# Optimization experiments

Hardware: AMD Instinct MI355X
Metric: run time of the kernel (lower is better)

Reference implementation:

```python
import jax, jax.numpy as jnp
import numpy as np

B, N, S, F = 16384, 1152, 576, 8  # batch, n_sites, n_symm, features
LOG2 = float(np.log(2.0))


def log_cosh(x):
    # numerically stable log(cosh(x)) = |x| + log1p(exp(-2|x|)) - log(2)
    a = jnp.abs(x)
    return a + jnp.log1p(jnp.exp(-2.0 * a)) - LOG2


def setup_inputs() -> dict:
    key = jax.random.key(0)
    ks = iter(jax.random.split(key, 32))
    f32 = jnp.float32
    d = {}
    d['x'] = jax.random.normal(next(ks), (B, N), dtype=f32)
    d['symmetries'] = jax.random.randint(next(ks), (S, N), 0, N, dtype=jnp.int32)
    d['corr0'] = jax.random.randint(next(ks), (576, 4), 0, N, dtype=jnp.int32)
    d['corr1'] = jax.random.randint(next(ks), (576, 4), 0, N, dtype=jnp.int32)
    d['corr2'] = jax.random.randint(next(ks), (24, 24), 0, N, dtype=jnp.int32)
    d['corr3'] = jax.random.randint(next(ks), (24, 24), 0, N, dtype=jnp.int32)
    d['corr0_symm'] = jax.random.randint(next(ks), (S, 576), 0, 576, dtype=jnp.int32)
    d['corr1_symm'] = jax.random.randint(next(ks), (S, 576), 0, 576, dtype=jnp.int32)
    d['corr2_symm'] = jax.random.randint(next(ks), (S, 24), 0, 24, dtype=jnp.int32)
    d['corr3_symm'] = jax.random.randint(next(ks), (S, 24), 0, 24, dtype=jnp.int32)
    std = 0.01
    d['hidden_bias'] = std * jax.random.normal(next(ks), (F,), dtype=f32)
    d['symm_kernel'] = std * jax.random.normal(next(ks), (F, N), dtype=f32)
    d['visible_bias'] = std * jax.random.normal(next(ks), (2,), dtype=f32)
    d['corr0_bias'] = std * jax.random.normal(next(ks), (1,), dtype=f32)
    d['corr0_kernel'] = std * jax.random.normal(next(ks), (F, 576), dtype=f32)
    d['corr1_bias'] = std * jax.random.normal(next(ks), (1,), dtype=f32)
    d['corr1_kernel'] = std * jax.random.normal(next(ks), (F, 576), dtype=f32)
    d['corr2_bias'] = std * jax.random.normal(next(ks), (1,), dtype=f32)
    d['corr2_kernel'] = std * jax.random.normal(next(ks), (F, 24), dtype=f32)
    d['corr3_bias'] = std * jax.random.normal(next(ks), (1,), dtype=f32)
    d['corr3_kernel'] = std * jax.random.normal(next(ks), (F, 24), dtype=f32)
    d['loop0_hidden_bias'] = std * jax.random.normal(next(ks), (F,), dtype=f32)
    d['loop0_kernel'] = std * jax.random.normal(next(ks), (F, 24), dtype=f32)
    d['loop1_hidden_bias'] = std * jax.random.normal(next(ks), (F,), dtype=f32)
    d['loop1_kernel'] = std * jax.random.normal(next(ks), (F, 24), dtype=f32)
    return d


def reference(x, symmetries, corr0, corr1, corr2, corr3,
              corr0_symm, corr1_symm, corr2_symm, corr3_symm,
              hidden_bias, symm_kernel, visible_bias,
              corr0_bias, corr0_kernel, corr1_bias, corr1_kernel,
              corr2_bias, corr2_kernel, corr3_bias, corr3_kernel,
              loop0_hidden_bias, loop0_kernel, loop1_hidden_bias, loop1_kernel):
    n_batch = x.shape[0]
    # symmetrized kernel: (F, S, N)
    K = jnp.take(symm_kernel, symmetries, axis=1)
    theta = jnp.einsum('bn,fsn->bfs', x, K)  # (B, F, S)
    theta = theta + hidden_bias[:, None]
    bias = jnp.sum(x.reshape(n_batch, -1, 2), axis=1) @ visible_bias  # (B,)

    correlators = [corr0, corr1, corr2, corr3]
    corr_symms = [corr0_symm, corr1_symm, corr2_symm, corr3_symm]
    corr_biases = [corr0_bias, corr1_bias, corr2_bias, corr3_bias]
    corr_kernels = [corr0_kernel, corr1_kernel, corr2_kernel, corr3_kernel]

    corr_values = []
    for corr, csym, cb, ck in zip(correlators, corr_symms, corr_biases, corr_kernels):
        ckk = jnp.take(ck, csym, axis=1)               # (F, S, C)
        cv = jnp.take(x, corr, axis=1).prod(axis=2)    # (B, C)
        corr_values.append(cv)
        theta = theta + jnp.einsum('bc,fsc->bfs', cv, ckk)
        bias = bias + cb * jnp.sum(cv, axis=1)

    out = jnp.sum(log_cosh(theta), axis=(1, 2))  # (B,)

    # last two correlators are loop correlators with dedicated hidden units
    loop_params = [(loop0_hidden_bias, loop0_kernel, corr2_symm, corr_values[2]),
                   (loop1_hidden_bias, loop1_kernel, corr3_symm, corr_values[3])]
    for lhb, lk, lsym, lv in loop_params:
        lkk = jnp.take(lk, lsym, axis=1)                      # (F, S, C)
        lt = jnp.einsum('bc,fsc->bfs', lv, lkk) + lhb[:, None]
        out = out + jnp.sum(log_cosh(lt), axis=(1, 2))

    return out + bias
```

## Files before the change

kernel.cpp:

```cpp
#include <hip/hip_runtime.h>
#include <math.h>

#define B_    16384
#define N_    1152
#define KPAD  2496
#define NKT   39
#define KLOOP 256
#define NOUT  4608
#define NT2   18
#define LOG2F_ 0.69314718055994530942f

typedef unsigned short ushort_t;
typedef __attribute__((ext_vector_type(8))) short short8;
typedef __attribute__((ext_vector_type(4))) float floatx4;

__device__ __forceinline__ float log_cosh_f(float t) {
    float a = fabsf(t);
    return a + __logf(1.0f + __expf(-2.0f * a)) - LOG2F_;
}
__device__ __forceinline__ ushort_t bf16_rne(float f) {
    unsigned int u = __float_as_uint(f);
    return (ushort_t)((u + 0x7fffu + ((u >> 16) & 1u)) >> 16);
}
__device__ __forceinline__ float bf16_to_f(ushort_t h) {
    return __uint_as_float(((unsigned int)h) << 16);
}

typedef __attribute__((address_space(1))) const unsigned int guint;
typedef __attribute__((address_space(3))) unsigned int luint;
__device__ __forceinline__ void gload16(const ushort_t* src, ushort_t* dst) {
    __builtin_amdgcn_global_load_lds((guint*)src, (luint*)dst, 16, 0, 0);
}

__global__ __launch_bounds__(256) void build_w(
    const int* __restrict__ symm,
    const int* __restrict__ c0s, const int* __restrict__ c1s,
    const int* __restrict__ c2s, const int* __restrict__ c3s,
    const float* __restrict__ sk,
    const float* __restrict__ ck0, const float* __restrict__ ck1,
    const float* __restrict__ ck2, const float* __restrict__ ck3,
    const float* __restrict__ l0k, const float* __restrict__ l1k,
    ushort_t* __restrict__ Wb, ushort_t* __restrict__ LWb)
{
    __shared__ int idx[2352];
    const int s = blockIdx.x;
    const int tid = threadIdx.x;
    for (int i = tid; i < 1152; i += 256) idx[i] = symm[s * N_ + i];
    for (int i = tid; i < 576; i += 256) idx[1152 + i] = c0s[s * 576 + i];
    for (int i = tid; i < 576; i += 256) idx[1728 + i] = c1s[s * 576 + i];
    if (tid < 24) idx[2304 + tid] = c2s[s * 24 + tid];
    else if (tid < 48) idx[2328 + (tid - 24)] = c3s[s * 24 + (tid - 24)];
    __syncthreads();
    for (int f = 0; f < 8; ++f) {
        ushort_t* wr = Wb + (size_t)(s * 8 + f) * KPAD;
        for (int k = tid; k < KPAD; k += 256) {
            ushort_t o;
            if (k < 1152)      o = bf16_rne(sk[f * N_ + idx[k]]);
            else if (k < 1728) o = bf16_rne(ck0[f * 576 + idx[k]]);
            else if (k < 2304) o = bf16_rne(ck1[f * 576 + idx[k]]);
            else if (k < 2448) {
                int q = k - 2304, g = q / 48, c = q - g * 48;
                float w = (c < 24) ? ck2[f * 24 + idx[2304 + c]]
                                   : ck3[f * 24 + idx[2328 + (c - 24)]];
                ushort_t hi = bf16_rne(w);
                o = (g < 2) ? hi : bf16_rne(w - bf16_to_f(hi));
            } else o = 0;
            wr[k] = o;
        }
        ushort_t* lr = LWb + (size_t)(s * 8 + f) * KLOOP;
        for (int k2 = tid; k2 < KLOOP; k2 += 256) {
            int j2 = k2 >> 7, q = k2 & 127;
            ushort_t o = 0;
            if (q < 72) {
                int g = q / 24, c = q - g * 24;
                float w = j2 ? l1k[f * 24 + idx[2328 + c]]
                             : l0k[f * 24 + idx[2304 + c]];
                ushort_t hi = bf16_rne(w);
                o = (g < 2) ? hi : bf16_rne(w - bf16_to_f(hi));
            }
            lr[k2] = o;
        }
    }
}

__global__ __launch_bounds__(256) void build_cv(
    const float* __restrict__ x,
    const int* __restrict__ corr0, const int* __restrict__ corr1,
    const int* __restrict__ corr2, const int* __restrict__ corr3,
    const float* __restrict__ vb,
    const float* __restrict__ cb0, const float* __restrict__ cb1,
    const float* __restrict__ cb2, const float* __restrict__ cb3,
    ushort_t* __restrict__ XA, ushort_t* __restrict__ CVL,
    float* __restrict__ initb)
{
    __shared__ float xs[N_];
    __shared__ float red[256];
    __shared__ float cvhi[48], cvlo[48];
    const int tid = threadIdx.x;
    const int b = blockIdx.x;
    ushort_t* xr = XA + (size_t)b * KPAD;

    float bias = 0.f;
    const float vb0 = vb[0], vb1 = vb[1];
    for (int i = tid; i < N_; i += 256) {
        float v = x[(size_t)b * N_ + i];
        xs[i] = v;
        bias += v * ((i & 1) ? vb1 : vb0);
        xr[i] = bf16_rne(v);
    }
    __syncthreads();
    float s0 = 0.f, s1 = 0.f, s2 = 0.f, s3 = 0.f;
    for (int c = tid; c < 576; c += 256) {
        const int* i0 = corr0 + c * 4;
        float p = xs[i0[0]] * xs[i0[1]] * xs[i0[2]] * xs[i0[3]];
        xr[1152 + c] = bf16_rne(p); s0 += p;
        const int* i1 = corr1 + c * 4;
        float q = xs[i1[0]] * xs[i1[1]] * xs[i1[2]] * xs[i1[3]];
        xr[1728 + c] = bf16_rne(q); s1 += q;
    }
    if (tid < 48) {
        int j2 = tid / 24, c = tid - j2 * 24;
        const int* ii = (j2 ? corr3 : corr2) + c * 24;
        float p = 1.f;
        for (int j = 0; j < 24; ++j) p *= xs[ii[j]];
        float hv = bf16_to_f(bf16_rne(p));
        cvhi[tid] = hv;
        cvlo[tid] = p - hv;
        if (j2) s3 = p; else s2 = p;
    }
    __syncthreads();
    for (int i = tid; i < KPAD - 2304; i += 256) {
        ushort_t o = 0;
        if (i < 144) {
            int g = i / 48, c = i - g * 48;
            o = bf16_rne(g == 1 ? cvlo[c] : cvhi[c]);
        }
        xr[2304 + i] = o;
    }
    ushort_t* cr = CVL + (size_t)b * KLOOP;
    for (int k2 = tid; k2 < KLOOP; k2 += 256) {
        int j2 = k2 >> 7, q = k2 & 127;
        ushort_t o = 0;
        if (q < 72) {
            int g = q / 24, c = q - g * 24;
            o = bf16_rne(g == 1 ? cvlo[j2 * 24 + c] : cvhi[j2 * 24 + c]);
        }
        cr[k2] = o;
    }
    bias += cb0[0] * s0 + cb1[0] * s1 + cb2[0] * s2 + cb3[0] * s3;
    red[tid] = bias;
    __syncthreads();
    for (int off = 128; off; off >>= 1) {
        if (tid < off) red[tid] += red[tid + off];
        __syncthreads();
    }
    if (tid == 0) initb[b] = red[0];
}

__global__ __launch_bounds__(512, 2) void mfma_gemm(
    const ushort_t* __restrict__ XA, const ushort_t* __restrict__ Wb,
    const ushort_t* __restrict__ CVL, const ushort_t* __restrict__ LWb,
    const float* __restrict__ hidden_bias,
    const float* __restrict__ l0hb, const float* __restrict__ l1hb,
    float* __restrict__ partials)
{
    __shared__ __align__(16) ushort_t sh[65536];

    const int tid = threadIdx.x;
    const int l = tid & 63, w = tid >> 6;
    const int wm = w >> 2, wn = w & 3;
    const int lrow = l & 15, lg = l >> 4;
    const int srow = l >> 2;
    const int sgr8 = ((l & 3) ^ ((srow >> 1) & 3)) * 8;

    const int bid = blockIdx.x;
    const int swz = (bid & 7) * 144 + (bid >> 3);
    const int nt = swz % NT2, bt = swz / NT2;
    const int n0 = nt * 256, b0 = bt * 256;

    const ushort_t* XAb  = XA  + (size_t)b0 * KPAD;
    const ushort_t* Wbb  = Wb  + (size_t)n0 * KPAD;
    const ushort_t* CVb  = CVL + (size_t)b0 * KLOOP;
    const ushort_t* LWbb = LWb + (size_t)n0 * KLOOP;

    floatx4 acc[8][4];
    short8 bfr[4];

    auto STG = [&](const ushort_t* g, int stride, int kg, int ldsOff) {
#pragma unroll
        for (int i = 0; i < 2; ++i) {
            const int r0 = i * 128 + w * 16;
            gload16(g + (size_t)(r0 + srow) * stride + kg + sgr8,
                    &sh[ldsOff + r0 * 32]);
        }
    };

    const int ga = (lg ^ ((lrow >> 1) & 3)) * 8;
    const int abase = (wm * 128 + lrow) * 32 + ga;
    const int bbase = (wn * 64 + lrow) * 32 + ga;

    auto PHASE = [&](int asrc, int bsrc, int mih,
                     const ushort_t* sg, int sstride, int skg, int sdst,
                     int vf) {
        short8 afb[4];
        if (mih == 0) {
#pragma unroll
            for (int ni = 0; ni < 4; ++ni)
                bfr[ni] = *(const short8*)&sh[bsrc + bbase + ni * 512];
        }
#pragma unroll
        for (int mi = 0; mi < 4; ++mi)
            afb[mi] = *(const short8*)&sh[asrc + abase + mih * 2048 + mi * 512];
        if (sg) STG(sg, sstride, skg, sdst);
        __builtin_amdgcn_sched_barrier(0);
        __builtin_amdgcn_s_barrier();
        asm volatile("s_waitcnt lgkmcnt(0)" ::: "memory");
        __builtin_amdgcn_sched_barrier(0);
        __builtin_amdgcn_s_setprio(1);
#pragma unroll
        for (int mi = 0; mi < 4; ++mi)
#pragma unroll
            for (int ni = 0; ni < 4; ++ni)
                acc[mih * 4 + mi][ni] = __builtin_amdgcn_mfma_f32_16x16x32_bf16(
                    afb[mi], bfr[ni], acc[mih * 4 + mi][ni], 0, 0, 0);
        __builtin_amdgcn_s_setprio(0);
        if (vf == 1) asm volatile("s_waitcnt vmcnt(4)" ::: "memory");
        else if (vf == 2) asm volatile("s_waitcnt vmcnt(0)" ::: "memory");
        __builtin_amdgcn_sched_barrier(0);
        __builtin_amdgcn_s_barrier();
    };

#pragma unroll
    for (int mi = 0; mi < 8; ++mi)
#pragma unroll
        for (int ni = 0; ni < 4; ++ni) acc[mi][ni] = (floatx4){0.f, 0.f, 0.f, 0.f};

    STG(XAb, KPAD, 0, 0);      STG(Wbb, KPAD, 0, 8192);
    STG(XAb, KPAD, 32, 16384); STG(Wbb, KPAD, 32, 24576);
    asm volatile("s_waitcnt vmcnt(4)" ::: "memory");
    __builtin_amdgcn_s_barrier();

#pragma unroll 1
    for (int t = 0; t < NKT - 1; ++t) {
        const int cb = (t & 1) * 32768, nb = cb ^ 32768;
        const int kg = (t + 1) * 64;
        PHASE(cb,         cb + 8192,  0, XAb, KPAD, kg,      nb,         0);
        PHASE(cb,         cb + 8192,  1, Wbb, KPAD, kg,      nb + 8192,  1);
        PHASE(cb + 16384, cb + 24576, 0, XAb, KPAD, kg + 32, nb + 16384, 0);
        PHASE(cb + 16384, cb + 24576, 1, Wbb, KPAD, kg + 32, nb + 24576, 1);
    }
    {
        PHASE(0,     8192,  0, nullptr, 0, 0, 0, 0);
        PHASE(0,     8192,  1, nullptr, 0, 0, 0, 2);
        PHASE(16384, 24576, 0, nullptr, 0, 0, 0, 0);
        PHASE(16384, 24576, 1, nullptr, 0, 0, 0, 0);
    }

    float rs[32];
    {
        const float hbv = hidden_bias[l & 7];
#pragma unroll
        for (int mi = 0; mi < 8; ++mi)
#pragma unroll
            for (int reg = 0; reg < 4; ++reg) {
                float t = 0.f;
#pragma unroll
                for (int ni = 0; ni < 4; ++ni)
                    t += log_cosh_f(acc[mi][ni][reg] + hbv);
                rs[mi * 4 + reg] = t;
            }
    }

#pragma unroll 1
    for (int j2 = 0; j2 < 2; ++j2) {
#pragma unroll
        for (int mi = 0; mi < 8; ++mi)
#pragma unroll
            for (int ni = 0; ni < 4; ++ni) acc[mi][ni] = (floatx4){0.f, 0.f, 0.f, 0.f};
        __syncthreads();
        const int kb = j2 * 128;
        STG(CVb, KLOOP, kb,      0);      STG(LWbb, KLOOP, kb,      8192);
        STG(CVb, KLOOP, kb + 32, 16384);  STG(LWbb, KLOOP, kb + 32, 24576);
        STG(CVb, KLOOP, kb + 64, 32768);  STG(LWbb, KLOOP, kb + 64, 40960);
        STG(CVb, KLOOP, kb + 96, 49152);  STG(LWbb, KLOOP, kb + 96, 57344);
        __syncthreads();
        PHASE(0,     8192,  0, nullptr, 0, 0, 0, 0);
        PHASE(0,     8192,  1, nullptr, 0, 0, 0, 0);
        PHASE(16384, 24576, 0, nullptr, 0, 0, 0, 0);
        PHASE(16384, 24576, 1, nullptr, 0, 0, 0, 0);
        PHASE(32768, 40960, 0, nullptr, 0, 0, 0, 0);
        PHASE(32768, 40960, 1, nullptr, 0, 0, 0, 0);
        PHASE(49152, 57344, 0, nullptr, 0, 0, 0, 0);
        PHASE(49152, 57344, 1, nullptr, 0, 0, 0, 0);
        const float lbv = (j2 ? l1hb : l0hb)[l & 7];
#pragma unroll
        for (int mi = 0; mi < 8; ++mi)
#pragma unroll
            for (int reg = 0; reg < 4; ++reg) {
                float t = 0.f;
#pragma unroll
                for (int ni = 0; ni < 4; ++ni)
                    t += log_cosh_f(acc[mi][ni][reg] + lbv);
                rs[mi * 4 + reg] += t;
            }
    }

    __syncthreads();
    float* red = (float*)sh;
#pragma unroll
    for (int mi = 0; mi < 8; ++mi)
#pragma unroll
        for (int reg = 0; reg < 4; ++reg) {
            float v = rs[mi * 4 + reg];
            v += __shfl_xor(v, 1);
            v += __shfl_xor(v, 2);
            v += __shfl_xor(v, 4);
            v += __shfl_xor(v, 8);
            if (lrow == 0)
                red[(wm * 128 + mi * 16 + lg * 4 + reg) * 5 + wn] = v;
        }
    __syncthreads();
    if (tid < 256) {
        float t = red[tid * 5 + 0] + red[tid * 5 + 1] +
                  red[tid * 5 + 2] + red[tid * 5 + 3];
        partials[(size_t)nt * B_ + b0 + tid] = t;
    }
}

__global__ __launch_bounds__(256) void finalize_out(
    const float* __restrict__ initb, const float* __restrict__ partials,
    float* __restrict__ out)
{
    int b = blockIdx.x * 256 + threadIdx.x;
    float s = initb[b];
#pragma unroll
    for (int t = 0; t < NT2; ++t) s += partials[(size_t)t * B_ + b];
    out[b] = s;
}

extern "C" void kernel_launch(void* const* d_in, const int* in_sizes, int n_in,
                              void* d_out, int out_size, void* d_ws, size_t ws_size,
                              hipStream_t stream) {
    const float* x    = (const float*)d_in[0];
    const int* symm   = (const int*)d_in[1];
    const int* corr0  = (const int*)d_in[2];
    const int* corr1  = (const int*)d_in[3];
    const int* corr2  = (const int*)d_in[4];
    const int* corr3  = (const int*)d_in[5];
    const int* c0s    = (const int*)d_in[6];
    const int* c1s    = (const int*)d_in[7];
    const int* c2s    = (const int*)d_in[8];
    const int* c3s    = (const int*)d_in[9];
    const float* hb   = (const float*)d_in[10];
    const float* sk   = (const float*)d_in[11];
    const float* vb   = (const float*)d_in[12];
    const float* cb0  = (const float*)d_in[13];
    const float* ck0  = (const float*)d_in[14];
    const float* cb1  = (const float*)d_in[15];
    const float* ck1  = (const float*)d_in[16];
    const float* cb2  = (const float*)d_in[17];
    const float* ck2  = (const float*)d_in[18];
    const float* cb3  = (const float*)d_in[19];
    const float* ck3  = (const float*)d_in[20];
    const float* l0hb = (const float*)d_in[21];
    const float* l0k  = (const float*)d_in[22];
    const float* l1hb = (const float*)d_in[23];
    const float* l1k  = (const float*)d_in[24];

    ushort_t* wsu = (ushort_t*)d_ws;
    ushort_t* Wb  = wsu;
    ushort_t* XA  = Wb + (size_t)NOUT * KPAD;
    ushort_t* LWb = XA + (size_t)B_ * KPAD;
    ushort_t* CVL = LWb + (size_t)NOUT * KLOOP;
    float* initb    = (float*)(CVL + (size_t)B_ * KLOOP);
    float* partials = initb + B_;

    build_w<<<576, 256, 0, stream>>>(
        symm, c0s, c1s, c2s, c3s, sk, ck0, ck1, ck2, ck3, l0k, l1k, Wb, LWb);
    build_cv<<<B_, 256, 0, stream>>>(
        x, corr0, corr1, corr2, corr3, vb, cb0, cb1, cb2, cb3, XA, CVL, initb);
    mfma_gemm<<<1152, 512, 0, stream>>>(
        XA, Wb, CVL, LWb, hb, l0hb, l1hb, partials);
    finalize_out<<<B_ / 256, 256, 0, stream>>>(initb, partials, (float*)d_out);
}
```

Baseline: 610.9 us.

## Halve GEMM M-tile to 128 rows with triple-buffered K=32 pipeline

Shrinks each GEMM block's batch tile from 256 to 128 rows, doubling the grid to 2304 blocks. The K-step drops from 64 to 32 with a three-stage rotating LDS buffer and one barrier per step. Accumulators are halved and launch bounds raised to 4 blocks per SM to increase occupancy and latency hiding. The cost is more reloading of the W operand from global memory and less MFMA work per LDS load. Reductions are also moved into a separate shared array, accumulated per phase rather than held in registers.

```diff
diff --git a/kernel.cpp b/kernel.cpp
--- a/kernel.cpp
+++ b/kernel.cpp
@@ -4,7 +4,7 @@
 #define B_    16384
 #define N_    1152
 #define KPAD  2496
-#define NKT   39
+#define NKT32 78
 #define KLOOP 256
 #define NOUT  4608
 #define NT2   18
@@ -157,14 +157,15 @@
     if (tid == 0) initb[b] = red[0];
 }
 
-__global__ __launch_bounds__(512, 2) void mfma_gemm(
+__global__ __launch_bounds__(512, 4) void mfma_gemm(
     const ushort_t* __restrict__ XA, const ushort_t* __restrict__ Wb,
     const ushort_t* __restrict__ CVL, const ushort_t* __restrict__ LWb,
     const float* __restrict__ hidden_bias,
     const float* __restrict__ l0hb, const float* __restrict__ l1hb,
     float* __restrict__ partials)
 {
-    __shared__ __align__(16) ushort_t sh[65536];
+    __shared__ __align__(16) ushort_t sh[36864];
+    __shared__ float redsh[640];
 
     const int tid = threadIdx.x;
     const int l = tid & 63, w = tid >> 6;
@@ -174,155 +175,139 @@
     const int sgr8 = ((l & 3) ^ ((srow >> 1) & 3)) * 8;
 
     const int bid = blockIdx.x;
-    const int swz = (bid & 7) * 144 + (bid >> 3);
-    const int nt = swz % NT2, bt = swz / NT2;
-    const int n0 = nt * 256, b0 = bt * 256;
+    const int swz = (bid & 7) * 288 + (bid >> 3);
+    const int nt = swz >> 7, bt = swz & 127;
+    const int n0 = nt * 256, b0 = bt * 128;
 
     const ushort_t* XAb  = XA  + (size_t)b0 * KPAD;
     const ushort_t* Wbb  = Wb  + (size_t)n0 * KPAD;
     const ushort_t* CVb  = CVL + (size_t)b0 * KLOOP;
     const ushort_t* LWbb = LWb + (size_t)n0 * KLOOP;
 
-    floatx4 acc[8][4];
-    short8 bfr[4];
-
-    auto STG = [&](const ushort_t* g, int stride, int kg, int ldsOff) {
+    floatx4 acc[4][4];
+
+    auto STGA = [&](const ushort_t* g, int stride, int kg, int bo) {
+        gload16(g + (size_t)(w * 16 + srow) * stride + kg + sgr8,
+                &sh[bo + w * 16 * 32]);
+    };
+    auto STGB = [&](const ushort_t* g, int stride, int kg, int bo) {
 #pragma unroll
         for (int i = 0; i < 2; ++i) {
             const int r0 = i * 128 + w * 16;
             gload16(g + (size_t)(r0 + srow) * stride + kg + sgr8,
-                    &sh[ldsOff + r0 * 32]);
+                    &sh[bo + 4096 + r0 * 32]);
         }
     };
 
     const int ga = (lg ^ ((lrow >> 1) & 3)) * 8;
-    const int abase = (wm * 128 + lrow) * 32 + ga;
-    const int bbase = (wn * 64 + lrow) * 32 + ga;
-
-    auto PHASE = [&](int asrc, int bsrc, int mih,
-                     const ushort_t* sg, int sstride, int skg, int sdst,
-                     int vf) {
-        short8 afb[4];
-        if (mih == 0) {
+    const int abase = (wm * 64 + lrow) * 32 + ga;
+    const int bbase = 4096 + (wn * 64 + lrow) * 32 + ga;
+
+    auto TILE = [&](int bo) {
+        short8 af[4], bfr[4];
+#pragma unroll
+        for (int mi = 0; mi < 4; ++mi)
+            af[mi] = *(const short8*)&sh[bo + abase + mi * 512];
+#pragma unroll
+        for (int ni = 0; ni < 4; ++ni)
+            bfr[ni] = *(const short8*)&sh[bo + bbase + ni * 512];
+        __builtin_amdgcn_s_setprio(1);
+#pragma unroll
+        for (int mi = 0; mi < 4; ++mi)
 #pragma unroll
             for (int ni = 0; ni < 4; ++ni)
-                bfr[ni] = *(const short8*)&sh[bsrc + bbase + ni * 512];
-        }
-#pragma unroll
-        for (int mi = 0; mi < 4; ++mi)
-            afb[mi] = *(const short8*)&sh[asrc + abase + mih * 2048 + mi * 512];
-        if (sg) STG(sg, sstride, skg, sdst);
-        __builtin_amdgcn_sched_barrier(0);
+                acc[mi][ni] = __builtin_amdgcn_mfma_f32_16x16x32_bf16(
+                    af[mi], bfr[ni], acc[mi][ni], 0, 0, 0);
+        __builtin_amdgcn_s_setprio(0);
+    };
+
+#pragma unroll
+    for (int mi = 0; mi < 4; ++mi)
+#pragma unroll
+        for (int ni = 0; ni < 4; ++ni) acc[mi][ni] = (floatx4){0.f, 0.f, 0.f, 0.f};
+
+    int c0 = 0, c1 = 12288, c2 = 24576;
+    STGA(XAb, KPAD, 0, c0);  STGB(Wbb, KPAD, 0, c0);
+    STGA(XAb, KPAD, 32, c1); STGB(Wbb, KPAD, 32, c1);
+#pragma unroll 1
+    for (int t = 0; t < NKT32 - 1; ++t) {
+        asm volatile("s_waitcnt vmcnt(3)" ::: "memory");
         __builtin_amdgcn_s_barrier();
-        asm volatile("s_waitcnt lgkmcnt(0)" ::: "memory");
-        __builtin_amdgcn_sched_barrier(0);
-        __builtin_amdgcn_s_setprio(1);
-#pragma unroll
-        for (int mi = 0; mi < 4; ++mi)
-#pragma unroll
-            for (int ni = 0; ni < 4; ++ni)
-                acc[mih * 4 + mi][ni] = __builtin_amdgcn_mfma_f32_16x16x32_bf16(
-                    afb[mi], bfr[ni], acc[mih * 4 + mi][ni], 0, 0, 0);
-        __builtin_amdgcn_s_setprio(0);
-        if (vf == 1) asm volatile("s_waitcnt vmcnt(4)" ::: "memory");
-        else if (vf == 2) asm volatile("s_waitcnt vmcnt(0)" ::: "memory");
-        __builtin_amdgcn_sched_barrier(0);
-        __builtin_amdgcn_s_barrier();
-    };
-
-#pragma unroll
-    for (int mi = 0; mi < 8; ++mi)
-#pragma unroll
-        for (int ni = 0; ni < 4; ++ni) acc[mi][ni] = (floatx4){0.f, 0.f, 0.f, 0.f};
-
-    STG(XAb, KPAD, 0, 0);      STG(Wbb, KPAD, 0, 8192);
-    STG(XAb, KPAD, 32, 16384); STG(Wbb, KPAD, 32, 24576);
-    asm volatile("s_waitcnt vmcnt(4)" ::: "memory");
+        if (t < NKT32 - 2) {
+            STGA(XAb, KPAD, (t + 2) * 32, c2);
+            STGB(Wbb, KPAD, (t + 2) * 32, c2);
+        }
+        TILE(c0);
+        int tmp = c0; c0 = c1; c1 = c2; c2 = tmp;
+    }
+    asm volatile("s_waitcnt vmcnt(0)" ::: "memory");
     __builtin_amdgcn_s_barrier();
-
-#pragma unroll 1
-    for (int t = 0; t < NKT - 1; ++t) {
-        const int cb = (t & 1) * 32768, nb = cb ^ 32768;
-        const int kg = (t + 1) * 64;
-        PHASE(cb,         cb + 8192,  0, XAb, KPAD, kg,      nb,         0);
-        PHASE(cb,         cb + 8192,  1, Wbb, KPAD, kg,      nb + 8192,  1);
-        PHASE(cb + 16384, cb + 24576, 0, XAb, KPAD, kg + 32, nb + 16384, 0);
-        PHASE(cb + 16384, cb + 24576, 1, Wbb, KPAD, kg + 32, nb + 24576, 1);
-    }
-    {
-        PHASE(0,     8192,  0, nullptr, 0, 0, 0, 0);
-        PHASE(0,     8192,  1, nullptr, 0, 0, 0, 2);
-        PHASE(16384, 24576, 0, nullptr, 0, 0, 0, 0);
-        PHASE(16384, 24576, 1, nullptr, 0, 0, 0, 0);
-    }
-
-    float rs[32];
+    TILE(c0);
+
     {
         const float hbv = hidden_bias[l & 7];
 #pragma unroll
-        for (int mi = 0; mi < 8; ++mi)
+        for (int mi = 0; mi < 4; ++mi)
 #pragma unroll
             for (int reg = 0; reg < 4; ++reg) {
-                float t = 0.f;
+                float v = 0.f;
 #pragma unroll
                 for (int ni = 0; ni < 4; ++ni)
-                    t += log_cosh_f(acc[mi][ni][reg] + hbv);
-                rs[mi * 4 + reg] = t;
+                    v += log_cosh_f(acc[mi][ni][reg] + hbv);
+                v += __shfl_xor(v, 1);
+                v += __shfl_xor(v, 2);
+                v += __shfl_xor(v, 4);
+                v += __shfl_xor(v, 8);
+                if (lrow == 0)
+                    redsh[(wm * 64 + mi * 16 + lg * 4 + reg) * 5 + wn] = v;
             }
     }
 
 #pragma unroll 1
     for (int j2 = 0; j2 < 2; ++j2) {
 #pragma unroll
-        for (int mi = 0; mi < 8; ++mi)
+        for (int mi = 0; mi < 4; ++mi)
 #pragma unroll
             for (int ni = 0; ni < 4; ++ni) acc[mi][ni] = (floatx4){0.f, 0.f, 0.f, 0.f};
         __syncthreads();
         const int kb = j2 * 128;
-        STG(CVb, KLOOP, kb,      0);      STG(LWbb, KLOOP, kb,      8192);
-        STG(CVb, KLOOP, kb + 32, 16384);  STG(LWbb, KLOOP, kb + 32, 24576);
-        STG(CVb, KLOOP, kb + 64, 32768);  STG(LWbb, KLOOP, kb + 64, 40960);
-        STG(CVb, KLOOP, kb + 96, 49152);  STG(LWbb, KLOOP, kb + 96, 57344);
-        __syncthreads();
-        PHASE(0,     8192,  0, nullptr, 0, 0, 0, 0);
-        PHASE(0,     8192,  1, nullptr, 0, 0, 0, 0);
-        PHASE(16384, 24576, 0, nullptr, 0, 0, 0, 0);
-        PHASE(16384, 24576, 1, nullptr, 0, 0, 0, 0);
-        PHASE(32768, 40960, 0, nullptr, 0, 0, 0, 0);
-        PHASE(32768, 40960, 1, nullptr, 0, 0, 0, 0);
-        PHASE(49152, 57344, 0, nullptr, 0, 0, 0, 0);
-        PHASE(49152, 57344, 1, nullptr, 0, 0, 0, 0);
+        STGA(CVb, KLOOP, kb, 0);          STGB(LWbb, KLOOP, kb, 0);
+        STGA(CVb, KLOOP, kb + 32, 12288); STGB(LWbb, KLOOP, kb + 32, 12288);
+        int m0 = 0, m1 = 12288, m2 = 24576;
+#pragma unroll 1
+        for (int t = 0; t < 4; ++t) {
+            if (t < 3) asm volatile("s_waitcnt vmcnt(3)" ::: "memory");
+            else       asm volatile("s_waitcnt vmcnt(0)" ::: "memory");
+            __builtin_amdgcn_s_barrier();
+            if (t < 2) {
+                STGA(CVb, KLOOP, kb + (t + 2) * 32, m2);
+                STGB(LWbb, KLOOP, kb + (t + 2) * 32, m2);
+            }
+            TILE(m0);
+            int tmp = m0; m0 = m1; m1 = m2; m2 = tmp;
+        }
         const float lbv = (j2 ? l1hb : l0hb)[l & 7];
 #pragma unroll
-        for (int mi = 0; mi < 8; ++mi)
+        for (int mi = 0; mi < 4; ++mi)
 #pragma unroll
             for (int reg = 0; reg < 4; ++reg) {
-                float t = 0.f;
+                float v = 0.f;
 #pragma unroll
                 for (int ni = 0; ni < 4; ++ni)
-                    t += log_cosh_f(acc[mi][ni][reg] + lbv);
-                rs[mi * 4 + reg] += t;
+                    v += log_cosh_f(acc[mi][ni][reg] + lbv);
+                v += __shfl_xor(v, 1);
+                v += __shfl_xor(v, 2);
+                v += __shfl_xor(v, 4);
+                v += __shfl_xor(v, 8);
+                if (lrow == 0)
+                    redsh[(wm * 64 + mi * 16 + lg * 4 + reg) * 5 + wn] += v;
             }
     }
 
     __syncthreads();
-    float* red = (float*)sh;
-#pragma unroll
-    for (int mi = 0; mi < 8; ++mi)
-#pragma unroll
-        for (int reg = 0; reg < 4; ++reg) {
-            float v = rs[mi * 4 + reg];
-            v += __shfl_xor(v, 1);
-            v += __shfl_xor(v, 2);
-            v += __shfl_xor(v, 4);
-            v += __shfl_xor(v, 8);
-            if (lrow == 0)
-                red[(wm * 128 + mi * 16 + lg * 4 + reg) * 5 + wn] = v;
-        }
-    __syncthreads();
-    if (tid < 256) {
-        float t = red[tid * 5 + 0] + red[tid * 5 + 1] +
-                  red[tid * 5 + 2] + red[tid * 5 + 3];
+    if (tid < 128) {
+        float t = redsh[tid * 5 + 0] + redsh[tid * 5 + 1] +
+                  redsh[tid * 5 + 2] + redsh[tid * 5 + 3];
         partials[(size_t)nt * B_ + b0 + tid] = t;
     }
 }
@@ -379,7 +364,7 @@
         symm, c0s, c1s, c2s, c3s, sk, ck0, ck1, ck2, ck3, l0k, l1k, Wb, LWb);
     build_cv<<<B_, 256, 0, stream>>>(
         x, corr0, corr1, corr2, corr3, vb, cb0, cb1, cb2, cb3, XA, CVL, initb);
-    mfma_gemm<<<1152, 512, 0, stream>>>(
+    mfma_gemm<<<2304, 512, 0, stream>>>(
         XA, Wb, CVL, LWb, hb, l0hb, l1hb, partials);
     finalize_out<<<B_ / 256, 256, 0, stream>>>(initb, partials, (float*)d_out);
 }
```

New measurement: 579.5 us. 5.1% less time.
